# Optimization experiments

Measured on AMD Instinct MI355X. Metric: run time of the kernel, lower is better.

The kernel has to match this reference:

```python
import jax, jax.numpy as jnp
import numpy as np

B, T, D, H, O = 32, 2048, 256, 512, 256


def setup_inputs() -> dict:
    key = jax.random.key(0)
    ks = jax.random.split(key, 6)
    x = jax.random.normal(ks[0], (B, T, D), dtype=jnp.float32)
    h0 = jax.random.normal(ks[1], (1, B, H), dtype=jnp.float32)
    # S, A stand in for orthogonal-initialized recurrent params
    S = jax.random.normal(ks[2], (H, H), dtype=jnp.float32) / np.sqrt(H).astype(np.float32)
    A = jax.random.normal(ks[3], (H, H), dtype=jnp.float32) / np.sqrt(H).astype(np.float32)
    lambda_raw = jnp.float32(0.0)  # logit(0.5)
    W_in = jax.random.normal(ks[4], (H, D), dtype=jnp.float32) / np.sqrt(D).astype(np.float32)
    b_in = jnp.zeros((H,), dtype=jnp.float32)
    W_out = jax.random.normal(ks[5], (O, H), dtype=jnp.float32) / np.sqrt(H).astype(np.float32)
    b_out = jnp.zeros((O,), dtype=jnp.float32)
    return {"x": x, "h0": h0, "S": S, "A": A, "lambda_raw": lambda_raw,
            "W_in": W_in, "b_in": b_in, "W_out": W_out, "b_out": b_out}


def reference(x, h0, S, A, lambda_raw, W_in, b_in, W_out, b_out):
    # Effective recurrent weight: W = lam * sym(S) + (1-lam) * asym(A)
    lam = jax.nn.sigmoid(lambda_raw)
    W = lam * (0.5 * (S + S.T)) + (1.0 - lam) * (0.5 * (A - A.T))  # [H, H]

    h_init = h0[0]  # [B, H]
    # Input projection for all timesteps at once: [B, T, H]
    xp = jnp.einsum('btd,hd->bth', x, W_in) + b_in

    def step(h, xt):
        # h: [B, H], xt: [B, H]
        h = jnp.tanh(xt + h @ W.T)
        y = jax.nn.softmax(h @ W_out.T + b_out, axis=-1)  # [B, O]
        return h, (y, h)

    _, (ys, hs) = jax.lax.scan(step, h_init, jnp.swapaxes(xp, 0, 1))  # [T,B,O], [T,B,H]
    return jnp.swapaxes(ys, 0, 1), jnp.swapaxes(hs, 0, 1)  # [B,T,O], [B,T,H]
```

## Files before the change

### kernel.cpp

```cpp
#include <hip/hip_runtime.h>

namespace {
constexpr int kH = 512, kD = 256, kO = 256, kB = 32, kT = 2048;
constexpr int kRows = kB * kT;
constexpr int kSlices = 8;
}

__global__ __launch_bounds__(256) void prep_kernel(
    const float* __restrict__ S, const float* __restrict__ A,
    const float* __restrict__ lam_raw, const float* __restrict__ W_in,
    const float* __restrict__ W_out, float* __restrict__ Wt,
    float* __restrict__ W_in_t, float* __restrict__ Wout_t) {
  const int idx = blockIdx.x * 256 + threadIdx.x;
  const float lam = 1.0f / (1.0f + __expf(-lam_raw[0]));
  if (idx < kH * kH) {
    const int k = idx >> 9, j = idx & (kH - 1);
    const float sym = 0.5f * (S[j * kH + k] + S[k * kH + j]);
    const float asym = 0.5f * (A[j * kH + k] - A[k * kH + j]);
    Wt[idx] = lam * sym + (1.0f - lam) * asym;
  }
  if (idx < kD * kH) {
    const int d = idx >> 9, h = idx & (kH - 1);
    W_in_t[idx] = W_in[h * kD + d];
  }
  if (idx < kH * kO) {
    const int h = idx >> 8, o = idx & (kO - 1);
    Wout_t[idx] = W_out[o * kH + h];
  }
}

template <int BM, int BN, int BK>
__global__ __launch_bounds__(256) void gemm_bias_kernel(
    const float* __restrict__ A, const float* __restrict__ Bt,
    const float* __restrict__ bias, float* __restrict__ C,
    int M, int N, int K) {
  __shared__ float As[BK][BM + 4];
  __shared__ float Bs[BK][BN];
  const int tid = threadIdx.x;
  const int m0 = blockIdx.x * BM, n0 = blockIdx.y * BN;
  const int ar = tid >> 2, ac = (tid & 3) << 2;
  const int br = tid >> 4, bc = (tid & 15) << 2;
  const int tx = tid & 15, ty = tid >> 4;
  float4 acc[8];
#pragma unroll
  for (int i = 0; i < 8; ++i) acc[i] = make_float4(0.f, 0.f, 0.f, 0.f);

  for (int k0 = 0; k0 < K; k0 += BK) {
    const float4 a0 = *(const float4*)&A[(long)(m0 + ar) * K + k0 + ac];
    const float4 a1 = *(const float4*)&A[(long)(m0 + ar + 64) * K + k0 + ac];
    const float4 b0 = *(const float4*)&Bt[(long)(k0 + br) * N + n0 + bc];
    __syncthreads();
    As[ac + 0][ar] = a0.x; As[ac + 1][ar] = a0.y;
    As[ac + 2][ar] = a0.z; As[ac + 3][ar] = a0.w;
    As[ac + 0][ar + 64] = a1.x; As[ac + 1][ar + 64] = a1.y;
    As[ac + 2][ar + 64] = a1.z; As[ac + 3][ar + 64] = a1.w;
    *(float4*)&Bs[br][bc] = b0;
    __syncthreads();
#pragma unroll
    for (int kk = 0; kk < BK; ++kk) {
      const float4 b4 = *(const float4*)&Bs[kk][tx * 4];
      const float4 va0 = *(const float4*)&As[kk][ty * 8];
      const float4 va1 = *(const float4*)&As[kk][ty * 8 + 4];
#define FMA_ROW(ACC, SV)                                                   \
      ACC.x += (SV) * b4.x; ACC.y += (SV) * b4.y;                          \
      ACC.z += (SV) * b4.z; ACC.w += (SV) * b4.w;
      FMA_ROW(acc[0], va0.x) FMA_ROW(acc[1], va0.y)
      FMA_ROW(acc[2], va0.z) FMA_ROW(acc[3], va0.w)
      FMA_ROW(acc[4], va1.x) FMA_ROW(acc[5], va1.y)
      FMA_ROW(acc[6], va1.z) FMA_ROW(acc[7], va1.w)
#undef FMA_ROW
    }
  }
  const float4 bv = *(const float4*)&bias[n0 + tx * 4];
#pragma unroll
  for (int mi = 0; mi < 8; ++mi) {
    float4 r;
    r.x = acc[mi].x + bv.x; r.y = acc[mi].y + bv.y;
    r.z = acc[mi].z + bv.z; r.w = acc[mi].w + bv.w;
    *(float4*)&C[(long)(m0 + ty * 8 + mi) * N + n0 + tx * 4] = r;
  }
}

__global__ __launch_bounds__(512, 1) void rnn_kernel(
    const float* __restrict__ Wt, const float* __restrict__ h0,
    float* __restrict__ hs, unsigned long long* __restrict__ hglob) {
  const int bid = blockIdx.x;
  const int b = bid >> 3;
  const int s = bid & 7;
  const int tid = threadIdx.x;
  const int j = tid & 63;
  const int kc = tid >> 6;
  const int jg = s * 64 + j;
  __shared__ float h_lds[kH];
  __shared__ float part[8 * 64];

  float wk[64];
  const float* wp = Wt + (long)(64 * kc) * kH + jg;
#pragma unroll
  for (int m = 0; m < 64; ++m) wk[m] = wp[(long)m * kH];

  float* hb = hs + (long)b * kT * kH;
  unsigned long long* hg = hglob + (long)b * 1024;

  for (int t = 0; t < kT; ++t) {
    float xpv = 0.f;
    if (kc == 0) xpv = hb[(long)t * kH + jg];

    if (t == 0) {
      h_lds[tid] = h0[b * kH + tid];
    } else {
      const int slot = t & 1;
      unsigned long long v;
      do {
        v = __hip_atomic_load(&hg[slot * 512 + tid], __ATOMIC_RELAXED,
                              __HIP_MEMORY_SCOPE_AGENT);
      } while ((unsigned)(v >> 32) != (unsigned)t);
      h_lds[tid] = __uint_as_float((unsigned)v);
    }
    __syncthreads();

    const float4* h4 = (const float4*)&h_lds[64 * kc];
    float a0 = 0.f, a1 = 0.f, a2 = 0.f, a3 = 0.f;
#pragma unroll
    for (int q = 0; q < 16; ++q) {
      const float4 hv = h4[q];
      a0 += wk[4 * q + 0] * hv.x;
      a1 += wk[4 * q + 1] * hv.y;
      a2 += wk[4 * q + 2] * hv.z;
      a3 += wk[4 * q + 3] * hv.w;
    }
    part[kc * 64 + j] = (a0 + a1) + (a2 + a3);
    __syncthreads();

    if (kc == 0) {
      float sum = xpv;
#pragma unroll
      for (int e = 0; e < 8; ++e) sum += part[e * 64 + j];
      const float hn = tanhf(sum);
      hb[(long)t * kH + jg] = hn;
      const unsigned long long pv =
          ((unsigned long long)(unsigned)(t + 1) << 32) | __float_as_uint(hn);
      __hip_atomic_store(&hg[((t + 1) & 1) * 512 + jg], pv, __ATOMIC_RELAXED,
                         __HIP_MEMORY_SCOPE_AGENT);
    }
  }
}

__global__ __launch_bounds__(256) void softmax_kernel(float* __restrict__ Z) {
  const int lane = threadIdx.x & 63;
  const int wid = threadIdx.x >> 6;
  const long row = (long)blockIdx.x * 4 + wid;
  float* z = Z + row * kO;
  float4 v = *(float4*)&z[lane * 4];
  float m = fmaxf(fmaxf(v.x, v.y), fmaxf(v.z, v.w));
#pragma unroll
  for (int off = 32; off > 0; off >>= 1) m = fmaxf(m, __shfl_xor(m, off));
  v.x = __expf(v.x - m); v.y = __expf(v.y - m);
  v.z = __expf(v.z - m); v.w = __expf(v.w - m);
  float ssum = v.x + v.y + v.z + v.w;
#pragma unroll
  for (int off = 32; off > 0; off >>= 1) ssum += __shfl_xor(ssum, off);
  const float r = 1.0f / ssum;
  v.x *= r; v.y *= r; v.z *= r; v.w *= r;
  *(float4*)&z[lane * 4] = v;
}

extern "C" void kernel_launch(void* const* d_in, const int* in_sizes, int n_in,
                              void* d_out, int out_size, void* d_ws, size_t ws_size,
                              hipStream_t stream) {
  const float* x     = (const float*)d_in[0];
  const float* h0    = (const float*)d_in[1];
  const float* S     = (const float*)d_in[2];
  const float* A     = (const float*)d_in[3];
  const float* lam   = (const float*)d_in[4];
  const float* W_in  = (const float*)d_in[5];
  const float* b_in  = (const float*)d_in[6];
  const float* W_out = (const float*)d_in[7];
  const float* b_out = (const float*)d_in[8];

  float* ys = (float*)d_out;
  float* hs = ys + (long)kB * kT * kO;

  float* Wt     = (float*)d_ws;
  float* W_in_t = Wt + kH * kH;
  float* Wout_t = W_in_t + kD * kH;
  unsigned long long* hglob = (unsigned long long*)W_in_t;

  prep_kernel<<<1024, 256, 0, stream>>>(S, A, lam, W_in, W_out, Wt, W_in_t, Wout_t);

  dim3 g2(kRows / 128, kH / 64);
  gemm_bias_kernel<128, 64, 16><<<g2, 256, 0, stream>>>(x, W_in_t, b_in, hs,
                                                        kRows, kH, kD);
  rnn_kernel<<<kB * kSlices, 512, 0, stream>>>(Wt, h0, hs, hglob);

  dim3 g4(kRows / 128, kO / 64);
  gemm_bias_kernel<128, 64, 16><<<g4, 256, 0, stream>>>(hs, Wout_t, b_out, ys,
                                                        kRows, kO, kH);
  softmax_kernel<<<kRows / 4, 256, 0, stream>>>(ys);
}
```

Before: 3.704 ms.

## Interleave two batch recurrences per block to hide cross-block exchange latency

The recurrent kernel now runs 128 blocks, each handling two batch elements (g and g+16) for its 64-column slice. It alternates the step for batch A and batch B, so the spin-wait on one batch's exchange overlaps with the other batch's compute. It also prefetches the next timestep's input projection and replaces tanhf with an exp-based fast tanh clamped to [-10, 10]. This halves the block count and doubles serial work per block, which could lengthen the critical path if the exchange latency is not actually hidden.

```diff
diff --git a/kernel.cpp b/kernel.cpp
--- a/kernel.cpp
+++ b/kernel.cpp
@@ -3,7 +3,6 @@
 namespace {
 constexpr int kH = 512, kD = 256, kO = 256, kB = 32, kT = 2048;
 constexpr int kRows = kB * kT;
-constexpr int kSlices = 8;
 }
 
 __global__ __launch_bounds__(256) void prep_kernel(
@@ -81,67 +80,113 @@
   }
 }
 
+__device__ __forceinline__ float fast_tanh(float x) {
+  x = fminf(fmaxf(x, -10.0f), 10.0f);
+  const float e = __expf(2.0f * x);
+  return (e - 1.0f) / (e + 1.0f);
+}
+
 __global__ __launch_bounds__(512, 1) void rnn_kernel(
     const float* __restrict__ Wt, const float* __restrict__ h0,
-    float* __restrict__ hs, unsigned long long* __restrict__ hglob) {
+    float* __restrict__ hs, unsigned long long* __restrict__ exch) {
   const int bid = blockIdx.x;
-  const int b = bid >> 3;
-  const int s = bid & 7;
+  const int g = bid & 15;
+  const int s = bid >> 4;
+  const int bA = g, bB = g + 16;
   const int tid = threadIdx.x;
   const int j = tid & 63;
   const int kc = tid >> 6;
   const int jg = s * 64 + j;
-  __shared__ float h_lds[kH];
-  __shared__ float part[8 * 64];
+
+  __shared__ float hA[kH], hB[kH];
+  __shared__ float pA[8 * 64], pB[8 * 64];
 
   float wk[64];
   const float* wp = Wt + (long)(64 * kc) * kH + jg;
 #pragma unroll
   for (int m = 0; m < 64; ++m) wk[m] = wp[(long)m * kH];
 
-  float* hb = hs + (long)b * kT * kH;
-  unsigned long long* hg = hglob + (long)b * 1024;
+  float* hbA = hs + (long)bA * kT * kH;
+  float* hbB = hs + (long)bB * kT * kH;
+  unsigned long long* hgA = exch + (long)bA * 1024;
+  unsigned long long* hgB = exch + (long)bB * 1024;
+
+  hA[tid] = h0[bA * kH + tid];
+  hB[tid] = h0[bB * kH + tid];
+  float xpA = 0.f, xpB = 0.f;
+  if (kc == 0) { xpA = hbA[jg]; xpB = hbB[jg]; }
+  __syncthreads();
 
   for (int t = 0; t < kT; ++t) {
-    float xpv = 0.f;
-    if (kc == 0) xpv = hb[(long)t * kH + jg];
-
-    if (t == 0) {
-      h_lds[tid] = h0[b * kH + tid];
-    } else {
-      const int slot = t & 1;
+    if (t > 0) {
+      unsigned long long* p = &hgA[(t & 1) * 512 + tid];
       unsigned long long v;
       do {
-        v = __hip_atomic_load(&hg[slot * 512 + tid], __ATOMIC_RELAXED,
-                              __HIP_MEMORY_SCOPE_AGENT);
+        v = __hip_atomic_load(p, __ATOMIC_RELAXED, __HIP_MEMORY_SCOPE_AGENT);
       } while ((unsigned)(v >> 32) != (unsigned)t);
-      h_lds[tid] = __uint_as_float((unsigned)v);
-    }
-    __syncthreads();
-
-    const float4* h4 = (const float4*)&h_lds[64 * kc];
-    float a0 = 0.f, a1 = 0.f, a2 = 0.f, a3 = 0.f;
-#pragma unroll
-    for (int q = 0; q < 16; ++q) {
-      const float4 hv = h4[q];
-      a0 += wk[4 * q + 0] * hv.x;
-      a1 += wk[4 * q + 1] * hv.y;
-      a2 += wk[4 * q + 2] * hv.z;
-      a3 += wk[4 * q + 3] * hv.w;
-    }
-    part[kc * 64 + j] = (a0 + a1) + (a2 + a3);
-    __syncthreads();
-
+      hA[tid] = __uint_as_float((unsigned)v);
+    }
+    __syncthreads();
+    {
+      const float4* h4 = (const float4*)&hA[64 * kc];
+      float a0 = 0.f, a1 = 0.f, a2 = 0.f, a3 = 0.f;
+#pragma unroll
+      for (int q = 0; q < 16; ++q) {
+        const float4 hv = h4[q];
+        a0 += wk[4 * q + 0] * hv.x;
+        a1 += wk[4 * q + 1] * hv.y;
+        a2 += wk[4 * q + 2] * hv.z;
+        a3 += wk[4 * q + 3] * hv.w;
+      }
+      pA[kc * 64 + j] = (a0 + a1) + (a2 + a3);
+    }
+    __syncthreads();
     if (kc == 0) {
-      float sum = xpv;
-#pragma unroll
-      for (int e = 0; e < 8; ++e) sum += part[e * 64 + j];
-      const float hn = tanhf(sum);
-      hb[(long)t * kH + jg] = hn;
-      const unsigned long long pv =
-          ((unsigned long long)(unsigned)(t + 1) << 32) | __float_as_uint(hn);
-      __hip_atomic_store(&hg[((t + 1) & 1) * 512 + jg], pv, __ATOMIC_RELAXED,
-                         __HIP_MEMORY_SCOPE_AGENT);
+      float sum = xpA;
+#pragma unroll
+      for (int e = 0; e < 8; ++e) sum += pA[e * 64 + j];
+      const float hn = fast_tanh(sum);
+      hbA[(long)t * kH + jg] = hn;
+      __hip_atomic_store(&hgA[((t + 1) & 1) * 512 + jg],
+                         ((unsigned long long)(unsigned)(t + 1) << 32) |
+                             __float_as_uint(hn),
+                         __ATOMIC_RELAXED, __HIP_MEMORY_SCOPE_AGENT);
+      xpA = (t + 1 < kT) ? hbA[(long)(t + 1) * kH + jg] : 0.f;
+    }
+    if (t > 0) {
+      unsigned long long* p = &hgB[(t & 1) * 512 + tid];
+      unsigned long long v;
+      do {
+        v = __hip_atomic_load(p, __ATOMIC_RELAXED, __HIP_MEMORY_SCOPE_AGENT);
+      } while ((unsigned)(v >> 32) != (unsigned)t);
+      hB[tid] = __uint_as_float((unsigned)v);
+    }
+    __syncthreads();
+    {
+      const float4* h4 = (const float4*)&hB[64 * kc];
+      float a0 = 0.f, a1 = 0.f, a2 = 0.f, a3 = 0.f;
+#pragma unroll
+      for (int q = 0; q < 16; ++q) {
+        const float4 hv = h4[q];
+        a0 += wk[4 * q + 0] * hv.x;
+        a1 += wk[4 * q + 1] * hv.y;
+        a2 += wk[4 * q + 2] * hv.z;
+        a3 += wk[4 * q + 3] * hv.w;
+      }
+      pB[kc * 64 + j] = (a0 + a1) + (a2 + a3);
+    }
+    __syncthreads();
+    if (kc == 0) {
+      float sum = xpB;
+#pragma unroll
+      for (int e = 0; e < 8; ++e) sum += pB[e * 64 + j];
+      const float hn = fast_tanh(sum);
+      hbB[(long)t * kH + jg] = hn;
+      __hip_atomic_store(&hgB[((t + 1) & 1) * 512 + jg],
+                         ((unsigned long long)(unsigned)(t + 1) << 32) |
+                             __float_as_uint(hn),
+                         __ATOMIC_RELAXED, __HIP_MEMORY_SCOPE_AGENT);
+      xpB = (t + 1 < kT) ? hbB[(long)(t + 1) * kH + jg] : 0.f;
     }
   }
 }
@@ -184,14 +229,15 @@
   float* Wt     = (float*)d_ws;
   float* W_in_t = Wt + kH * kH;
   float* Wout_t = W_in_t + kD * kH;
-  unsigned long long* hglob = (unsigned long long*)W_in_t;
+
+  unsigned long long* exch = (unsigned long long*)W_in_t;
 
   prep_kernel<<<1024, 256, 0, stream>>>(S, A, lam, W_in, W_out, Wt, W_in_t, Wout_t);
 
   dim3 g2(kRows / 128, kH / 64);
   gemm_bias_kernel<128, 64, 16><<<g2, 256, 0, stream>>>(x, W_in_t, b_in, hs,
                                                         kRows, kH, kD);
-  rnn_kernel<<<kB * kSlices, 512, 0, stream>>>(Wt, h0, hs, hglob);
+  rnn_kernel<<<128, 512, 0, stream>>>(Wt, h0, hs, exch);
 
   dim3 g4(kRows / 128, kO / 64);
   gemm_bias_kernel<128, 64, 16><<<g4, 256, 0, stream>>>(hs, Wout_t, b_out, ys,
```

Result: slower. 4.516 ms (+21.9%).
